# Optimization experiments

Hardware: AMD Instinct MI355X
Metric: run time of the kernel (lower is better)

## Reference

```python
import jax, jax.numpy as jnp
import numpy as np

TEMPERATURE = 12.5   # init temperature
SINKHORN_EPS = 0.05  # entropic regularization replacing exact cv2.EMD LP solve
SINKHORN_ITERS = 100 # fixed iteration count (jit-friendly)


def _weight_vector(A, B):
    # A: [M,C,H,W], B: [N,C,H,W] -> [M, N, H*W]
    # matches: global-avg-pool B over HW, inner product over channels per spatial node of A
    Bp = B.mean(axis=(2, 3))                      # [N, C]
    comb = jnp.einsum('mchw,nc->mnhw', A, Bp)     # [M, N, H, W]
    comb = comb.reshape(A.shape[0], B.shape[0], -1)
    return jax.nn.relu(comb) + 0.001


def _center(x):
    # norm='center': subtract channel mean (dim 1)
    return x - x.mean(axis=1, keepdims=True)


def _similarity_map(support, query):
    # metric='cosine': sim[q, w, i, j] = cos(query[q,:,i], support[w,:,j]) over channels
    s = support.reshape(support.shape[0], support.shape[1], -1)  # [W, C, Ns]
    q = query.reshape(query.shape[0], query.shape[1], -1)        # [Q, C, Nq]
    s = s / jnp.maximum(jnp.linalg.norm(s, axis=1, keepdims=True), 1e-8)
    q = q / jnp.maximum(jnp.linalg.norm(q, axis=1, keepdims=True), 1e-8)
    return jnp.einsum('qci,wcj->qwij', q, s)                     # [Q, W, Nq, Ns]


def _sinkhorn_flow(cost, a, b, eps=SINKHORN_EPS, n_iters=SINKHORN_ITERS):
    # Batched entropic OT in log-space. cost: [..., n, m]; a: [..., n]; b: [..., m].
    log_a = jnp.log(a)
    log_b = jnp.log(b)
    logK = -cost / eps

    def body(_, uv):
        u, v = uv
        u = log_a - jax.nn.logsumexp(logK + v[..., None, :], axis=-1)
        v = log_b - jax.nn.logsumexp(logK + u[..., None], axis=-2)
        return (u, v)

    u0 = jnp.zeros_like(log_a)
    v0 = jnp.zeros_like(log_b)
    u, v = jax.lax.fori_loop(0, n_iters, body, (u0, v0))
    return jnp.exp(logK + u[..., None] + v[..., None, :])  # transport plan [..., n, m]


def setup_inputs() -> dict:
    key = jax.random.key(0)
    k1, k2 = jax.random.split(key)
    support = jax.random.normal(k1, (32, 512, 8, 8), dtype=jnp.float32)
    query = jax.random.normal(k2, (256, 512, 8, 8), dtype=jnp.float32)
    return {"support": support, "query": query}


def reference(support, query):
    # weight_1: [Q, W, N] (row/query-node marginals), weight_2: [W, Q, N] (col/support-node)
    w1 = _weight_vector(query, support)
    w2 = _weight_vector(support, query)

    s = _center(support)
    q = _center(query)
    sim = _similarity_map(s, q)  # [Q, W, N, N]

    num_node = w1.shape[-1]
    # opencv path: relu (no-op, already >0) + 1e-5, rescale so each marginal sums to num_node
    a = w1 + 1e-5
    a = a * (num_node / a.sum(-1, keepdims=True))              # [Q, W, N]
    b = jnp.transpose(w2, (1, 0, 2)) + 1e-5                    # weight_2[j, i] -> [Q, W, N]
    b = b * (num_node / b.sum(-1, keepdims=True))

    flow = _sinkhorn_flow(1.0 - sim, a, b)                     # [Q, W, N, N]
    flow = jax.lax.stop_gradient(flow)  # opencv flow is a non-differentiable constant

    logits = (sim * flow).sum((-1, -2)) * (TEMPERATURE / num_node)  # [Q, W]
    return logits
```

## Files before the change

### kernel.cpp

```cpp
#include <hip/hip_runtime.h>
#include <math.h>


#define DEV static __device__ __forceinline__

typedef _Float16 half8 __attribute__((ext_vector_type(8)));
typedef float floatx4 __attribute__((ext_vector_type(4)));

DEV float fast_rcp(float x) {
#if __has_builtin(__builtin_amdgcn_rcpf)
    return __builtin_amdgcn_rcpf(x);
#else
    return 1.0f / x;
#endif
}
DEV float fexp2(float x) {
#if __has_builtin(__builtin_amdgcn_exp2f)
    return __builtin_amdgcn_exp2f(x);
#else
    return exp2f(x);
#endif
}
DEV float flog2(float x) {
#if __has_builtin(__builtin_amdgcn_logf)
    return __builtin_amdgcn_logf(x);
#else
    return log2f(x);
#endif
}

#define K_SIM2M 28.853900817779268f
#define K_M2SIM 0.034657359027997264f
#define LDP 68

__global__ void __launch_bounds__(1024, 1)
norm_kernel(const float* __restrict__ support, const float* __restrict__ query,
            _Float16* __restrict__ Vht, _Float16* __restrict__ Uht,
            float* __restrict__ BpT, float* __restrict__ QpT,
            float* __restrict__ muA, float* __restrict__ nrmA,
            float* __restrict__ Ssc) {
    __shared__ float red1[16][64];
    __shared__ float red2[16][64];
    __shared__ float muL[64], invL[64];
    __shared__ float tile[128][65];

    int sid = blockIdx.x;
    const float* src;
    _Float16* dst;
    float* poolT;
    int pstride, pidx;
    if (sid < 32) {
        src = support + (size_t)sid * 32768; dst = Vht + (size_t)sid * 32768;
        poolT = BpT; pstride = 32; pidx = sid;
    } else {
        src = query + (size_t)(sid - 32) * 32768; dst = Uht + (size_t)(sid - 32) * 32768;
        poolT = QpT; pstride = 256; pidx = sid - 32;
    }

    int node = threadIdx.x & 63;
    int cq   = threadIdx.x >> 6;

    float s1 = 0.f, s2 = 0.f;
#pragma unroll 8
    for (int j = 0; j < 32; ++j) {
        int c = cq * 32 + j;
        float x = src[c * 64 + node];
        s1 += x; s2 += x * x;
        float ps = x;
        ps += __shfl_xor(ps, 1);  ps += __shfl_xor(ps, 2);  ps += __shfl_xor(ps, 4);
        ps += __shfl_xor(ps, 8);  ps += __shfl_xor(ps, 16); ps += __shfl_xor(ps, 32);
        if (node == 0) poolT[(size_t)c * pstride + pidx] = ps * (1.0f / 64.0f);
    }
    red1[cq][node] = s1;
    red2[cq][node] = s2;
    __syncthreads();
    if (threadIdx.x < 64) {
        float t1 = 0.f, t2 = 0.f;
#pragma unroll
        for (int k = 0; k < 16; ++k) { t1 += red1[k][node]; t2 += red2[k][node]; }
        float mu  = t1 * (1.0f / 512.0f);
        float ss  = t2 - 512.0f * mu * mu;
        float nrm = fmaxf(sqrtf(fmaxf(ss, 0.0f)), 1e-8f);
        muL[node]  = mu;
        invL[node] = 1.0f / nrm;
        muA[sid * 64 + node]  = mu;
        nrmA[sid * 64 + node] = nrm;
        float sS = t1;
        sS += __shfl_xor(sS, 1);  sS += __shfl_xor(sS, 2);  sS += __shfl_xor(sS, 4);
        sS += __shfl_xor(sS, 8);  sS += __shfl_xor(sS, 16); sS += __shfl_xor(sS, 32);
        if (node == 0) Ssc[sid] = sS * (1.0f / 64.0f);
    }
    __syncthreads();

    float mu = muL[node], inv = invL[node];
    for (int ch = 0; ch < 4; ++ch) {
#pragma unroll
        for (int j = 0; j < 8; ++j) {
            int cl = cq * 8 + j;
            float x = src[(ch * 128 + cl) * 64 + node];
            tile[cl][node] = (x - mu) * inv;
        }
        __syncthreads();
        {
            int g    = threadIdx.x;
            int slot = g & 63;
            int t    = (g >> 6) & 3;
            int kkl  = g >> 8;
            int nd   = t * 16 + (slot & 15);
            int c8   = (kkl << 2) | (slot >> 4);
            half8 v;
#pragma unroll
            for (int i = 0; i < 8; ++i) v[i] = (_Float16)tile[c8 * 8 + i][nd];
            *(half8*)(dst + ((size_t)ch * 1024 + g) * 8) = v;
        }
        __syncthreads();
    }
}

__global__ void __launch_bounds__(256)
marg_kernel(const _Float16* __restrict__ Uht, const _Float16* __restrict__ Vht,
            const float* __restrict__ BpT, const float* __restrict__ QpT,
            const float* __restrict__ muA, const float* __restrict__ nrmA,
            const float* __restrict__ Ssc,
            float* __restrict__ a_out, float* __restrict__ b_out) {
    __shared__ __align__(16) float WL[512 * 32];
    __shared__ float Sl[32];
    int lane = threadIdx.x & 63;
    int kq   = threadIdx.x >> 6;

    const _Float16* src16;
    float mu, nrm;
    if (blockIdx.x < 256) {
        int q = (blockIdx.x & 7) * 32 + (blockIdx.x >> 3);
        for (int t = threadIdx.x; t < 4096; t += 256)
            ((float4*)WL)[t] = ((const float4*)BpT)[t];
        if (threadIdx.x < 32) Sl[threadIdx.x] = Ssc[threadIdx.x];
        src16 = Uht + (size_t)q * 32768;
        mu  = muA[(32 + q) * 64 + lane];
        nrm = nrmA[(32 + q) * 64 + lane];
    } else {
        int id = blockIdx.x - 256;
        int w = id >> 3, qg = id & 7;
        for (int t = threadIdx.x; t < 4096; t += 256) {
            int c = t >> 3, k = t & 7;
            ((float4*)WL)[t] = ((const float4*)(QpT + (size_t)c * 256 + qg * 32))[k];
        }
        if (threadIdx.x < 32) Sl[threadIdx.x] = Ssc[32 + qg * 32 + threadIdx.x];
        src16 = Vht + (size_t)w * 32768;
        mu  = muA[w * 64 + lane];
        nrm = nrmA[w * 64 + lane];
    }
    __syncthreads();

    int lbase = (lane >> 4) * 64 + (lane & 15);
    float acc[8] = {0, 0, 0, 0, 0, 0, 0, 0};
#pragma unroll 1
    for (int kk = 0; kk < 16; ++kk) {
#pragma unroll
        for (int hi = 0; hi < 4; ++hi) {
            half8 x8 = *(const half8*)(src16 +
                        ((size_t)(kk * 256 + lbase + (hi << 4)) * 8));
            int cb = kk * 32 + hi * 8;
#pragma unroll
            for (int j = 0; j < 8; ++j) {
                float xv = (float)x8[j];
                const float* wl = WL + (cb + j) * 32 + kq * 8;
                float4 b0 = *(const float4*)wl;
                float4 b1 = *(const float4*)(wl + 4);
                acc[0] = fmaf(xv, b0.x, acc[0]); acc[1] = fmaf(xv, b0.y, acc[1]);
                acc[2] = fmaf(xv, b0.z, acc[2]); acc[3] = fmaf(xv, b0.w, acc[3]);
                acc[4] = fmaf(xv, b1.x, acc[4]); acc[5] = fmaf(xv, b1.y, acc[5]);
                acc[6] = fmaf(xv, b1.z, acc[6]); acc[7] = fmaf(xv, b1.w, acc[7]);
            }
        }
    }
#pragma unroll
    for (int k = 0; k < 8; ++k) {
        float raw = fmaf(mu, Sl[kq * 8 + k], nrm * acc[k]);
        float v = fmaxf(raw, 0.0f) + 0.001f;
        v += 1e-5f;
        float s = v;
        s += __shfl_xor(s, 1);  s += __shfl_xor(s, 2);  s += __shfl_xor(s, 4);
        s += __shfl_xor(s, 8);  s += __shfl_xor(s, 16); s += __shfl_xor(s, 32);
        v = v * (64.0f / s);
        if (blockIdx.x < 256) {
            int q = (blockIdx.x & 7) * 32 + (blockIdx.x >> 3), w = kq * 8 + k;
            a_out[((size_t)q * 32 + w) * 64 + lane] = v;
        } else {
            int id = blockIdx.x - 256;
            int w = id >> 3, q = (id & 7) * 32 + kq * 8 + k;
            b_out[((size_t)w * 256 + q) * 64 + lane] = v;
        }
    }
}

__global__ void __launch_bounds__(256, 4)
emd_kernel(const _Float16* __restrict__ Uht, const _Float16* __restrict__ Vht,
           const float* __restrict__ a_arr, const float* __restrict__ b_arr,
           float* __restrict__ out) {
    __shared__ __align__(16) float T[2][64 * LDP];

    int x    = blockIdx.x & 7;
    int i    = blockIdx.x >> 3;
    int w    = i & 31;
    int wave = threadIdx.x >> 6;
    int lane = threadIdx.x & 63;
    int q    = (x * 8 + (i >> 5)) * 4 + wave;
    int lo16 = lane & 15;
    int hi4  = lane >> 4;
    int ig   = lane >> 3;
    int jg   = lane & 7;

    floatx4 acc[4][4];
#pragma unroll
    for (int tm = 0; tm < 4; ++tm)
#pragma unroll
        for (int tn = 0; tn < 4; ++tn)
            acc[tm][tn] = (floatx4){0.f, 0.f, 0.f, 0.f};

    const _Float16* Abase = Uht + (size_t)q * 32768 + lane * 8;
    const _Float16* Bbase = Vht + (size_t)w * 32768 + lane * 8;
#pragma unroll 1
    for (int kk = 0; kk < 16; ++kk) {
        half8 bf[4];
#pragma unroll
        for (int t = 0; t < 4; ++t)
            bf[t] = *(const half8*)(Bbase + (size_t)(kk * 4 + t) * 512);
#pragma unroll
        for (int tm = 0; tm < 4; ++tm) {
            half8 af = *(const half8*)(Abase + (size_t)(kk * 4 + tm) * 512);
#pragma unroll
            for (int tn = 0; tn < 4; ++tn)
                acc[tm][tn] = __builtin_amdgcn_mfma_f32_16x16x32_f16(
                    af, bf[tn], acc[tm][tn], 0, 0, 0);
        }
    }

    float lmax = -2.0f;
#pragma unroll
    for (int tm = 0; tm < 4; ++tm)
#pragma unroll
        for (int tn = 0; tn < 4; ++tn)
#pragma unroll
            for (int r = 0; r < 4; ++r) lmax = fmaxf(lmax, acc[tm][tn][r]);
    lmax = fmaxf(lmax, __shfl_xor(lmax, 1));
    lmax = fmaxf(lmax, __shfl_xor(lmax, 2));
    lmax = fmaxf(lmax, __shfl_xor(lmax, 4));
    lmax = fmaxf(lmax, __shfl_xor(lmax, 8));
    lmax = fmaxf(lmax, __shfl_xor(lmax, 16));
    lmax = fmaxf(lmax, __shfl_xor(lmax, 32));
    float s0 = lmax;

    half8 Mh[8];
#pragma unroll 1
    for (int round = 0; round < 2; ++round) {
        if ((wave >> 1) == round) {
            float* buf = T[wave & 1];
#pragma unroll
            for (int tm = 0; tm < 4; ++tm)
#pragma unroll
                for (int tn = 0; tn < 4; ++tn)
#pragma unroll
                    for (int r = 0; r < 4; ++r) {
                        int row = tm * 16 + hi4 * 4 + r;
                        int col = tn * 16 + lo16;
                        int sp  = (col & 7) ^ (row >> 3);
                        buf[row * LDP + (col & ~7) + sp] =
                            fexp2((acc[tm][tn][r] - s0) * K_SIM2M);
                    }
        }
        __syncthreads();
        if ((wave >> 1) == round) {
            const float* buf = T[wave & 1];
#pragma unroll
            for (int t = 0; t < 8; ++t) {
                const float* p = buf + (ig * 8 + (jg ^ t)) * LDP + jg * 8;
                float4 m0 = *(const float4*)p;
                float4 m1 = *(const float4*)(p + 4);
                half8 h;
                h[0] = (_Float16)m0.x; h[1] = (_Float16)m0.y;
                h[2] = (_Float16)m0.z; h[3] = (_Float16)m0.w;
                h[4] = (_Float16)m1.x; h[5] = (_Float16)m1.y;
                h[6] = (_Float16)m1.z; h[7] = (_Float16)m1.w;
                Mh[t] = h;
            }
        }
        __syncthreads();
    }

    int gp = q * 32 + w;
    float a_own = a_arr[(size_t)gp * 64 + ig * 8 + jg];
    float b_own = b_arr[((size_t)w * 256 + q) * 64 + jg * 8 + ig];

    float wvp[8];
#pragma unroll
    for (int s = 0; s < 8; ++s) wvp[s] = 1.0f;
    float q8[8];
    float w_prev = -1.f;

#pragma unroll 1
    for (int it = 0; it < 100; ++it) {
        float p[8];
#pragma unroll
        for (int t = 0; t < 8; ++t) {
            float s = (float)Mh[t][0] * wvp[0];
#pragma unroll
            for (int c = 1; c < 8; ++c) s = fmaf((float)Mh[t][c], wvp[c], s);
            p[t] = s;
        }
        p[0] += __shfl_xor(p[4], 4); p[1] += __shfl_xor(p[5], 4);
        p[2] += __shfl_xor(p[6], 4); p[3] += __shfl_xor(p[7], 4);
        p[0] += __shfl_xor(p[2], 2); p[1] += __shfl_xor(p[3], 2);
        p[0] += __shfl_xor(p[1], 1);
        float z_own = a_own * fast_rcp(p[0]);
        q8[0] = z_own;
        q8[1] = __shfl_xor(q8[0], 1);
        q8[2] = __shfl_xor(q8[0], 2); q8[3] = __shfl_xor(q8[1], 2);
        q8[4] = __shfl_xor(q8[0], 4); q8[5] = __shfl_xor(q8[1], 4);
        q8[6] = __shfl_xor(q8[2], 4); q8[7] = __shfl_xor(q8[3], 4);
        float cp[8];
#pragma unroll
        for (int s = 0; s < 8; ++s) {
            float v = (float)Mh[0][s] * q8[0];
#pragma unroll
            for (int t = 1; t < 8; ++t) v = fmaf((float)Mh[t][s], q8[t], v);
            cp[s] = v;
        }
        cp[0] += __shfl_xor(cp[4], 32); cp[1] += __shfl_xor(cp[5], 32);
        cp[2] += __shfl_xor(cp[6], 32); cp[3] += __shfl_xor(cp[7], 32);
        cp[0] += __shfl_xor(cp[2], 16); cp[1] += __shfl_xor(cp[3], 16);
        cp[0] += __shfl_xor(cp[1], 8);
        float w_own = b_own * fast_rcp(cp[0]);
        wvp[0] = w_own;
        wvp[1] = __shfl_xor(wvp[0], 8);
        wvp[2] = __shfl_xor(wvp[0], 16); wvp[3] = __shfl_xor(wvp[1], 16);
        wvp[4] = __shfl_xor(wvp[0], 32); wvp[5] = __shfl_xor(wvp[1], 32);
        wvp[6] = __shfl_xor(wvp[2], 32); wvp[7] = __shfl_xor(wvp[3], 32);
        bool same = fabsf(w_own - w_prev) <= 1e-5f * w_own;
        w_prev = w_own;
        if (__all(same)) break;
    }

    float s = 0.f;
#pragma unroll
    for (int t = 0; t < 8; ++t)
#pragma unroll
        for (int c = 0; c < 8; ++c) {
            float m    = fmaxf((float)Mh[t][c], 1e-30f);
            float sim  = fmaf(flog2(m), K_M2SIM, s0);
            float flow = q8[t] * m * wvp[c];
            s = fmaf(sim, flow, s);
        }
    s += __shfl_xor(s, 1);  s += __shfl_xor(s, 2);  s += __shfl_xor(s, 4);
    s += __shfl_xor(s, 8);  s += __shfl_xor(s, 16); s += __shfl_xor(s, 32);
    if (lane == 0) out[gp] = s * 0.1953125f;
}

extern "C" void kernel_launch(void* const* d_in, const int* in_sizes, int n_in,
                              void* d_out, int out_size, void* d_ws, size_t ws_size,
                              hipStream_t stream) {
    (void)in_sizes; (void)n_in; (void)out_size; (void)ws_size;
    const float* support = (const float*)d_in[0];
    const float* query   = (const float*)d_in[1];

    char* ws = (char*)d_ws;
    _Float16* Uht = (_Float16*)ws;
    _Float16* Vht = Uht + 8388608;
    float* BpT  = (float*)(Vht + 1048576);
    float* QpT  = BpT + 16384;
    float* aA   = QpT + 131072;
    float* bA   = aA + 524288;
    float* muA  = bA + 524288;
    float* nrmA = muA + 18432;
    float* Ssc  = nrmA + 18432;

    norm_kernel<<<288, 1024, 0, stream>>>(support, query, Vht, Uht, BpT, QpT,
                                          muA, nrmA, Ssc);
    marg_kernel<<<512, 256, 0, stream>>>(Uht, Vht, BpT, QpT, muA, nrmA, Ssc,
                                         aA, bA);
    emd_kernel<<<2048, 256, 0, stream>>>(Uht, Vht, aA, bA, (float*)d_out);
}
```

Measured before the change: 183.7 us.

## Derive OT marginals from the cosine-similarity tile inside the EMD kernel

```diff
diff --git a/kernel.cpp b/kernel.cpp
--- a/kernel.cpp
+++ b/kernel.cpp
@@ -36,7 +36,6 @@
 __global__ void __launch_bounds__(1024, 1)
 norm_kernel(const float* __restrict__ support, const float* __restrict__ query,
             _Float16* __restrict__ Vht, _Float16* __restrict__ Uht,
-            float* __restrict__ BpT, float* __restrict__ QpT,
             float* __restrict__ muA, float* __restrict__ nrmA,
             float* __restrict__ Ssc) {
     __shared__ float red1[16][64];
@@ -47,14 +46,10 @@
     int sid = blockIdx.x;
     const float* src;
     _Float16* dst;
-    float* poolT;
-    int pstride, pidx;
     if (sid < 32) {
         src = support + (size_t)sid * 32768; dst = Vht + (size_t)sid * 32768;
-        poolT = BpT; pstride = 32; pidx = sid;
     } else {
         src = query + (size_t)(sid - 32) * 32768; dst = Uht + (size_t)(sid - 32) * 32768;
-        poolT = QpT; pstride = 256; pidx = sid - 32;
     }
 
     int node = threadIdx.x & 63;
@@ -66,10 +61,6 @@
         int c = cq * 32 + j;
         float x = src[c * 64 + node];
         s1 += x; s2 += x * x;
-        float ps = x;
-        ps += __shfl_xor(ps, 1);  ps += __shfl_xor(ps, 2);  ps += __shfl_xor(ps, 4);
-        ps += __shfl_xor(ps, 8);  ps += __shfl_xor(ps, 16); ps += __shfl_xor(ps, 32);
-        if (node == 0) poolT[(size_t)c * pstride + pidx] = ps * (1.0f / 64.0f);
     }
     red1[cq][node] = s1;
     red2[cq][node] = s2;
@@ -117,87 +108,10 @@
     }
 }
 
-__global__ void __launch_bounds__(256)
-marg_kernel(const _Float16* __restrict__ Uht, const _Float16* __restrict__ Vht,
-            const float* __restrict__ BpT, const float* __restrict__ QpT,
-            const float* __restrict__ muA, const float* __restrict__ nrmA,
-            const float* __restrict__ Ssc,
-            float* __restrict__ a_out, float* __restrict__ b_out) {
-    __shared__ __align__(16) float WL[512 * 32];
-    __shared__ float Sl[32];
-    int lane = threadIdx.x & 63;
-    int kq   = threadIdx.x >> 6;
-
-    const _Float16* src16;
-    float mu, nrm;
-    if (blockIdx.x < 256) {
-        int q = (blockIdx.x & 7) * 32 + (blockIdx.x >> 3);
-        for (int t = threadIdx.x; t < 4096; t += 256)
-            ((float4*)WL)[t] = ((const float4*)BpT)[t];
-        if (threadIdx.x < 32) Sl[threadIdx.x] = Ssc[threadIdx.x];
-        src16 = Uht + (size_t)q * 32768;
-        mu  = muA[(32 + q) * 64 + lane];
-        nrm = nrmA[(32 + q) * 64 + lane];
-    } else {
-        int id = blockIdx.x - 256;
-        int w = id >> 3, qg = id & 7;
-        for (int t = threadIdx.x; t < 4096; t += 256) {
-            int c = t >> 3, k = t & 7;
-            ((float4*)WL)[t] = ((const float4*)(QpT + (size_t)c * 256 + qg * 32))[k];
-        }
-        if (threadIdx.x < 32) Sl[threadIdx.x] = Ssc[32 + qg * 32 + threadIdx.x];
-        src16 = Vht + (size_t)w * 32768;
-        mu  = muA[w * 64 + lane];
-        nrm = nrmA[w * 64 + lane];
-    }
-    __syncthreads();
-
-    int lbase = (lane >> 4) * 64 + (lane & 15);
-    float acc[8] = {0, 0, 0, 0, 0, 0, 0, 0};
-#pragma unroll 1
-    for (int kk = 0; kk < 16; ++kk) {
-#pragma unroll
-        for (int hi = 0; hi < 4; ++hi) {
-            half8 x8 = *(const half8*)(src16 +
-                        ((size_t)(kk * 256 + lbase + (hi << 4)) * 8));
-            int cb = kk * 32 + hi * 8;
-#pragma unroll
-            for (int j = 0; j < 8; ++j) {
-                float xv = (float)x8[j];
-                const float* wl = WL + (cb + j) * 32 + kq * 8;
-                float4 b0 = *(const float4*)wl;
-                float4 b1 = *(const float4*)(wl + 4);
-                acc[0] = fmaf(xv, b0.x, acc[0]); acc[1] = fmaf(xv, b0.y, acc[1]);
-                acc[2] = fmaf(xv, b0.z, acc[2]); acc[3] = fmaf(xv, b0.w, acc[3]);
-                acc[4] = fmaf(xv, b1.x, acc[4]); acc[5] = fmaf(xv, b1.y, acc[5]);
-                acc[6] = fmaf(xv, b1.z, acc[6]); acc[7] = fmaf(xv, b1.w, acc[7]);
-            }
-        }
-    }
-#pragma unroll
-    for (int k = 0; k < 8; ++k) {
-        float raw = fmaf(mu, Sl[kq * 8 + k], nrm * acc[k]);
-        float v = fmaxf(raw, 0.0f) + 0.001f;
-        v += 1e-5f;
-        float s = v;
-        s += __shfl_xor(s, 1);  s += __shfl_xor(s, 2);  s += __shfl_xor(s, 4);
-        s += __shfl_xor(s, 8);  s += __shfl_xor(s, 16); s += __shfl_xor(s, 32);
-        v = v * (64.0f / s);
-        if (blockIdx.x < 256) {
-            int q = (blockIdx.x & 7) * 32 + (blockIdx.x >> 3), w = kq * 8 + k;
-            a_out[((size_t)q * 32 + w) * 64 + lane] = v;
-        } else {
-            int id = blockIdx.x - 256;
-            int w = id >> 3, q = (id & 7) * 32 + kq * 8 + k;
-            b_out[((size_t)w * 256 + q) * 64 + lane] = v;
-        }
-    }
-}
-
 __global__ void __launch_bounds__(256, 4)
 emd_kernel(const _Float16* __restrict__ Uht, const _Float16* __restrict__ Vht,
-           const float* __restrict__ a_arr, const float* __restrict__ b_arr,
-           float* __restrict__ out) {
+           const float* __restrict__ muA, const float* __restrict__ nrmA,
+           const float* __restrict__ Ssc, float* __restrict__ out) {
     __shared__ __align__(16) float T[2][64 * LDP];
 
     int x    = blockIdx.x & 7;
@@ -251,7 +165,20 @@
     lmax = fmaxf(lmax, __shfl_xor(lmax, 32));
     float s0 = lmax;
 
+    float nw[8], nu[8];
+#pragma unroll
+    for (int s = 0; s < 8; ++s) nw[s] = nrmA[w * 64 + (jg * 8 + (ig ^ s))];
+#pragma unroll
+    for (int t = 0; t < 8; ++t) nu[t] = nrmA[(32 + q) * 64 + (ig * 8 + (jg ^ t))];
+    float muR = muA[(32 + q) * 64 + (ig * 8 + jg)];
+    float muC = muA[w * 64 + (jg * 8 + ig)];
+    float Sw  = Ssc[w];
+    float Sq  = Ssc[32 + q];
+
     half8 Mh[8];
+    float pa[8], cb[8];
+#pragma unroll
+    for (int s = 0; s < 8; ++s) cb[s] = 0.f;
 #pragma unroll 1
     for (int round = 0; round < 2; ++round) {
         if ((wave >> 1) == round) {
@@ -265,8 +192,7 @@
                         int row = tm * 16 + hi4 * 4 + r;
                         int col = tn * 16 + lo16;
                         int sp  = (col & 7) ^ (row >> 3);
-                        buf[row * LDP + (col & ~7) + sp] =
-                            fexp2((acc[tm][tn][r] - s0) * K_SIM2M);
+                        buf[row * LDP + (col & ~7) + sp] = acc[tm][tn][r];
                     }
         }
         __syncthreads();
@@ -277,20 +203,46 @@
                 const float* p = buf + (ig * 8 + (jg ^ t)) * LDP + jg * 8;
                 float4 m0 = *(const float4*)p;
                 float4 m1 = *(const float4*)(p + 4);
+                float mm[8] = {m0.x, m0.y, m0.z, m0.w, m1.x, m1.y, m1.z, m1.w};
+                float s = mm[0] * nw[0];
+#pragma unroll
+                for (int c = 1; c < 8; ++c) s = fmaf(mm[c], nw[c], s);
+                pa[t] = s;
+#pragma unroll
+                for (int c = 0; c < 8; ++c) cb[c] = fmaf(mm[c], nu[t], cb[c]);
                 half8 h;
-                h[0] = (_Float16)m0.x; h[1] = (_Float16)m0.y;
-                h[2] = (_Float16)m0.z; h[3] = (_Float16)m0.w;
-                h[4] = (_Float16)m1.x; h[5] = (_Float16)m1.y;
-                h[6] = (_Float16)m1.z; h[7] = (_Float16)m1.w;
+#pragma unroll
+                for (int c = 0; c < 8; ++c)
+                    h[c] = (_Float16)fexp2((mm[c] - s0) * K_SIM2M);
                 Mh[t] = h;
             }
         }
         __syncthreads();
     }
 
-    int gp = q * 32 + w;
-    float a_own = a_arr[(size_t)gp * 64 + ig * 8 + jg];
-    float b_own = b_arr[((size_t)w * 256 + q) * 64 + jg * 8 + ig];
+    pa[0] += __shfl_xor(pa[4], 4); pa[1] += __shfl_xor(pa[5], 4);
+    pa[2] += __shfl_xor(pa[6], 4); pa[3] += __shfl_xor(pa[7], 4);
+    pa[0] += __shfl_xor(pa[2], 2); pa[1] += __shfl_xor(pa[3], 2);
+    pa[0] += __shfl_xor(pa[1], 1);
+    cb[0] += __shfl_xor(cb[4], 32); cb[1] += __shfl_xor(cb[5], 32);
+    cb[2] += __shfl_xor(cb[6], 32); cb[3] += __shfl_xor(cb[7], 32);
+    cb[0] += __shfl_xor(cb[2], 16); cb[1] += __shfl_xor(cb[3], 16);
+    cb[0] += __shfl_xor(cb[1], 8);
+
+    float araw = fmaf(muR, Sw, nu[0] * pa[0] * 0.015625f);
+    float braw = fmaf(muC, Sq, nw[0] * cb[0] * 0.015625f);
+
+    float va = fmaxf(araw, 0.0f) + 0.001f;  va += 1e-5f;
+    float sa = va;
+    sa += __shfl_xor(sa, 1);  sa += __shfl_xor(sa, 2);  sa += __shfl_xor(sa, 4);
+    sa += __shfl_xor(sa, 8);  sa += __shfl_xor(sa, 16); sa += __shfl_xor(sa, 32);
+    float a_own = va * (64.0f / sa);
+
+    float vb = fmaxf(braw, 0.0f) + 0.001f;  vb += 1e-5f;
+    float sb = vb;
+    sb += __shfl_xor(sb, 1);  sb += __shfl_xor(sb, 2);  sb += __shfl_xor(sb, 4);
+    sb += __shfl_xor(sb, 8);  sb += __shfl_xor(sb, 16); sb += __shfl_xor(sb, 32);
+    float b_own = vb * (64.0f / sb);
 
     float wvp[8];
 #pragma unroll
@@ -353,7 +305,7 @@
         }
     s += __shfl_xor(s, 1);  s += __shfl_xor(s, 2);  s += __shfl_xor(s, 4);
     s += __shfl_xor(s, 8);  s += __shfl_xor(s, 16); s += __shfl_xor(s, 32);
-    if (lane == 0) out[gp] = s * 0.1953125f;
+    if (lane == 0) out[q * 32 + w] = s * 0.1953125f;
 }
 
 extern "C" void kernel_launch(void* const* d_in, const int* in_sizes, int n_in,
@@ -366,17 +318,12 @@
     char* ws = (char*)d_ws;
     _Float16* Uht = (_Float16*)ws;
     _Float16* Vht = Uht + 8388608;
-    float* BpT  = (float*)(Vht + 1048576);
-    float* QpT  = BpT + 16384;
-    float* aA   = QpT + 131072;
-    float* bA   = aA + 524288;
-    float* muA  = bA + 524288;
+    float* muA  = (float*)(Vht + 1048576);
     float* nrmA = muA + 18432;
     float* Ssc  = nrmA + 18432;
 
-    norm_kernel<<<288, 1024, 0, stream>>>(support, query, Vht, Uht, BpT, QpT,
+    norm_kernel<<<288, 1024, 0, stream>>>(support, query, Vht, Uht,
                                           muA, nrmA, Ssc);
-    marg_kernel<<<512, 256, 0, stream>>>(Uht, Vht, BpT, QpT, muA, nrmA, Ssc,
-                                         aA, bA);
-    emd_kernel<<<2048, 256, 0, stream>>>(Uht, Vht, aA, bA, (float*)d_out);
-}
+    emd_kernel<<<2048, 256, 0, stream>>>(Uht, Vht, muA, nrmA, Ssc,
+                                         (float*)d_out);
+}
```

Result: slower. 242.2 us (+31.9%).
